# Kernel optimization log

Hardware: AMD Instinct MI355X
Metric: run time of the kernel (lower is better)

Reference implementation:

```python
import jax, jax.numpy as jnp
import numpy as np

# dims
B, N = 8, 16384
MODEL_DIM = 256
F = 32        # feature_dim
H = 4         # num_heads
G = 32        # grid_size
G3 = G * G * G
EPS = 1e-5


def setup_inputs() -> dict:
    key = jax.random.key(0)
    ks = jax.random.split(key, 9)
    eye = jnp.broadcast_to(jnp.eye(3, dtype=jnp.float32), (H, 3, 3))
    return {
        "input_tensor": jax.random.normal(ks[0], (B, MODEL_DIM, N), dtype=jnp.float32),
        "original_points": jax.random.normal(ks[1], (B, 3, N), dtype=jnp.float32),
        # Conv1d kernel_size=1, no bias -> plain (out,in) matmul weight
        "W_kv": jax.random.normal(ks[2], (H * (F + 3), MODEL_DIM), dtype=jnp.float32) * 0.02,
        # key BN affine (orig init weight=0; use small random to exercise path)
        "key_gamma": jax.random.normal(ks[3], (H * 3,), dtype=jnp.float32) * 0.1,
        "key_beta": jax.random.normal(ks[4], (H * 3,), dtype=jnp.float32) * 0.1,
        "val_gamma": 1.0 + jax.random.normal(ks[5], (H * F,), dtype=jnp.float32) * 0.1,
        "val_beta": jax.random.normal(ks[6], (H * F,), dtype=jnp.float32) * 0.1,
        # VolTransformer: per-head affine (rotation-ish matrix + translation)
        "R": eye + jax.random.normal(ks[7], (H, 3, 3), dtype=jnp.float32) * 0.05,
        "t": jax.random.normal(ks[8], (H, 3), dtype=jnp.float32) * 0.1,
    }


def _bn(x, gamma, beta):
    # training-mode BatchNorm1d over (batch, length) per channel; x: (B, C, N)
    mean = jnp.mean(x, axis=(0, 2), keepdims=True)
    var = jnp.var(x, axis=(0, 2), keepdims=True)
    xhat = (x - mean) * jax.lax.rsqrt(var + EPS)
    return xhat * gamma[None, :, None] + beta[None, :, None]


def reference(input_tensor, original_points, W_kv, key_gamma, key_beta,
              val_gamma, val_beta, R, t):
    # 1x1 conv == channel matmul: (B, H*(F+3), N)
    kv = jnp.einsum('om,bmn->bon', W_kv, input_tensor)
    keys_offset = _bn(kv[:, :H * 3], key_gamma, key_beta)          # (B, H*3, N)
    values = _bn(kv[:, H * 3:], val_gamma, val_beta)               # (B, H*F, N)

    keys_offset = keys_offset.reshape(B, H, 3, N)
    pts = original_points[:, None, :, :] + keys_offset             # (B,H,3,N)
    # per-head affine transform (VolTransformer)
    tk = jnp.einsum('hij,bhjn->bhin', R, pts) + t[None, :, :, None]
    lattice = jnp.tanh(tk)                                         # in (-1,1)

    # DifferentiablePositions: map (-1,1) -> [0, G-1], lower corner + local frac
    pos = (lattice + 1.0) * (0.5 * (G - 1))                        # (B,H,3,N)
    idx0 = jnp.clip(jnp.floor(pos), 0.0, G - 2).astype(jnp.int32)  # (B,H,3,N)
    local = pos - idx0                                             # (B,H,3,N)

    values_t = values.reshape(B, H, F, N).transpose(0, 1, 3, 2)    # (B,H,N,F)
    bh_off = (jnp.arange(B * H, dtype=jnp.int32).reshape(B, H) * G3)[:, :, None]

    out = jnp.zeros((B * H * G3, F), dtype=values.dtype)
    # trilinear splat-scatter over the 8 grid corners
    for cx in (0, 1):
        wx = local[:, :, 0] if cx else 1.0 - local[:, :, 0]
        for cy in (0, 1):
            wy = local[:, :, 1] if cy else 1.0 - local[:, :, 1]
            for cz in (0, 1):
                wz = local[:, :, 2] if cz else 1.0 - local[:, :, 2]
                w = wx * wy * wz                                    # (B,H,N)
                flat = ((idx0[:, :, 0] + cx) * G + (idx0[:, :, 1] + cy)) * G \
                       + (idx0[:, :, 2] + cz)                       # (B,H,N)
                seg = (bh_off + flat).reshape(-1)                   # (B*H*N,)
                data = (values_t * w[..., None]).reshape(-1, F)
                out = out + jax.ops.segment_sum(data, seg, num_segments=B * H * G3)

    # (B, H*F, G, G, G)
    return out.reshape(B, H, G3, F).transpose(0, 1, 3, 2).reshape(B, H * F, G, G, G)
```

## Files before the change

### kernel.cpp

```cpp
#include <hip/hip_runtime.h>
#include <cstddef>

#define Bz 8
#define Nn 16384
#define MD 256
#define Ff 32
#define Hh 4
#define Gg 32
#define G3v 32768
#define CKV 140
#define NG 32
#define NBX 31
#define NBY 31
#define NBZ 31
#define NB2 953312
#define NCH 931

using bf16x8 = __attribute__((ext_vector_type(8))) short;
using f32x16 = __attribute__((ext_vector_type(16))) float;

__device__ __forceinline__ unsigned bf16rne(float f) {
    unsigned u = __float_as_uint(f);
    return (u + 0x7fffu + ((u >> 16) & 1u)) >> 16;
}
__device__ __forceinline__ unsigned pk_bf16(float lo, float hi) {
    return bf16rne(lo) | (bf16rne(hi) << 16);
}

__global__ __launch_bounds__(256) void prep_w_kernel(const float* __restrict__ W,
                                                     unsigned short* __restrict__ Wbf)
{
    const int idx = blockIdx.x * 256 + threadIdx.x;
    const int e    = idx & 7;
    const int rest = idx >> 3;
    const int m    = rest % 160;
    const int kg   = rest / 160;
    const int k    = (kg << 3) + e;
    Wbf[idx] = (m < CKV) ? (unsigned short)bf16rne(W[m * MD + k]) : (unsigned short)0;
}

__global__ __launch_bounds__(256, 3) void gemm_stats_kernel(
    const float* __restrict__ X, const unsigned short* __restrict__ Wbf,
    float* __restrict__ vals, float* __restrict__ keys,
    float* __restrict__ gsum, float* __restrict__ gsq)
{
    __shared__ unsigned XlU[4096];
    __shared__ unsigned WlU[5120];
    __shared__ float red[280];

    const int bid = blockIdx.x;
    const int b   = bid >> 7;
    const int n0  = (bid & 127) << 7;
    const int t   = threadIdx.x;
    const int w    = t >> 6;
    const int ln   = t & 31;
    const int hi   = (t >> 5) & 1;

    f32x16 acc[5];
    #pragma unroll
    for (int mt = 0; mt < 5; ++mt)
        #pragma unroll
        for (int j = 0; j < 16; ++j) acc[mt][j] = 0.f;

    for (int ks = 0; ks < 4; ++ks) {
        const int k0 = ks << 6;
        if (ks > 0) __syncthreads();

        #pragma unroll
        for (int it = 0; it < 4; ++it) {
            const int a  = t + (it << 8);
            const int kp = a >> 5;
            const int n4 = (a & 31) << 2;
            const float4 r0 = *reinterpret_cast<const float4*>(
                X + (size_t)(b * MD + k0 + 2 * kp) * Nn + n0 + n4);
            const float4 r1 = *reinterpret_cast<const float4*>(
                X + (size_t)(b * MD + k0 + 2 * kp + 1) * Nn + n0 + n4);
            const int base = ((kp >> 2) << 9) + (n4 << 2) + (kp & 3);
            XlU[base]      = pk_bf16(r0.x, r1.x);
            XlU[base + 4]  = pk_bf16(r0.y, r1.y);
            XlU[base + 8]  = pk_bf16(r0.z, r1.z);
            XlU[base + 12] = pk_bf16(r0.w, r1.w);
        }
        {
            const unsigned* src = reinterpret_cast<const unsigned*>(Wbf) + ks * 5120;
            #pragma unroll
            for (int i = 0; i < 5; ++i) {
                const int d4 = (t + (i << 8)) << 2;
                *reinterpret_cast<uint4*>(&WlU[d4]) =
                    *reinterpret_cast<const uint4*>(&src[d4]);
            }
        }
        __syncthreads();

        const short* xs = reinterpret_cast<const short*>(XlU);
        const short* ws = reinterpret_cast<const short*>(WlU);
        #pragma unroll
        for (int kk = 0; kk < 4; ++kk) {
            const int grp = (kk << 1) + hi;
            const bf16x8 bf = *reinterpret_cast<const bf16x8*>(
                xs + (((grp << 7) + (w << 5) + ln) << 3));
            #pragma unroll
            for (int mt = 0; mt < 5; ++mt) {
                const bf16x8 af = *reinterpret_cast<const bf16x8*>(
                    ws + ((grp * 160 + (mt << 5) + ln) << 3));
                acc[mt] = __builtin_amdgcn_mfma_f32_32x32x16_bf16(af, bf, acc[mt], 0, 0, 0);
            }
        }
    }

    const int n = n0 + (w << 5) + ln;
    #pragma unroll
    for (int mt = 0; mt < 5; ++mt)
        #pragma unroll
        for (int reg = 0; reg < 16; ++reg) {
            const int ml = (reg & 3) + ((reg >> 2) << 3) + (hi << 2);
            const int c  = mt * 32 + ml;
            const float v = acc[mt][reg];
            if (c < 12) {
                const int hh = c / 3, kk2 = c - (c / 3) * 3;
                keys[(size_t)((b * Hh + hh) * 3 + kk2) * Nn + n] = v;
            } else if (c < CKV) {
                const int cv = c - 12;
                vals[((size_t)(b * Hh + (cv >> 5)) * Nn + n) * Ff + (cv & 31)] = v;
            }
        }

    red[t] = 0.f;
    if (t < 24) red[256 + t] = 0.f;
    __syncthreads();
    #pragma unroll
    for (int mt = 0; mt < 5; ++mt)
        #pragma unroll
        for (int reg = 0; reg < 16; ++reg) {
            if (mt == 4 && reg >= 8) continue;
            const int ml = (reg & 3) + ((reg >> 2) << 3) + (hi << 2);
            const int c  = mt * 32 + ml;
            float s = acc[mt][reg];
            float q = s * s;
            #pragma unroll
            for (int off = 1; off < 32; off <<= 1) {
                s += __shfl_xor(s, off);
                q += __shfl_xor(q, off);
            }
            if (ln == 0 && c < CKV) {
                atomicAdd(&red[c], s);
                atomicAdd(&red[140 + c], q);
            }
        }
    __syncthreads();
    if (t < CKV) {
        atomicAdd(&gsum[t], red[t]);
        atomicAdd(&gsq[t],  red[140 + t]);
    }
}

__global__ void finalize_kernel(const float* __restrict__ gsum, const float* __restrict__ gsq,
                                const float* __restrict__ kg, const float* __restrict__ kb,
                                const float* __restrict__ vg, const float* __restrict__ vb,
                                float* __restrict__ scale, float* __restrict__ shift)
{
    const int c = threadIdx.x;
    if (c < CKV) {
        const float inv = 1.f / (float)(Bz * Nn);
        const float m = gsum[c] * inv;
        const float v = fmaf(-m, m, gsq[c] * inv);
        float ga, be;
        if (c < 12) { ga = kg[c]; be = kb[c]; }
        else        { ga = vg[c - 12]; be = vb[c - 12]; }
        const float sc = ga * rsqrtf(v + 1e-5f);
        scale[c] = sc;
        shift[c] = fmaf(-m, sc, be);
    }
}

__global__ __launch_bounds__(256) void points_kernel(
    const float* __restrict__ keys, const float* __restrict__ orig,
    const float* __restrict__ Rm, const float* __restrict__ tv,
    const float* __restrict__ scale, const float* __restrict__ shift,
    float4* __restrict__ rec, int* __restrict__ cnt)
{
    const int bid = blockIdx.x;
    const int g   = bid >> 6;
    const int b   = g >> 2;
    const int h   = g & 3;
    const int t   = threadIdx.x;
    const int n   = ((bid & 63) << 8) + t;

    __shared__ float sR[9], st3[3], ksc[3], ksh[3];
    if (t < 9)       sR[t] = Rm[h * 9 + t];
    else if (t < 12) st3[t - 9] = tv[h * 3 + (t - 9)];
    else if (t < 15) { ksc[t - 12] = scale[h * 3 + (t - 12)];
                       ksh[t - 12] = shift[h * 3 + (t - 12)]; }
    __syncthreads();

    const float k0 = fmaf(keys[(size_t)(g * 3 + 0) * Nn + n], ksc[0], ksh[0]);
    const float k1 = fmaf(keys[(size_t)(g * 3 + 1) * Nn + n], ksc[1], ksh[1]);
    const float k2 = fmaf(keys[(size_t)(g * 3 + 2) * Nn + n], ksc[2], ksh[2]);
    const float p0 = orig[(size_t)(b * 3 + 0) * Nn + n] + k0;
    const float p1 = orig[(size_t)(b * 3 + 1) * Nn + n] + k1;
    const float p2 = orig[(size_t)(b * 3 + 2) * Nn + n] + k2;

    int   idx[3];
    float loc[3];
    #pragma unroll
    for (int d = 0; d < 3; ++d) {
        const float tk = fmaf(sR[d*3+0], p0, fmaf(sR[d*3+1], p1, fmaf(sR[d*3+2], p2, st3[d])));
        const float la = tanhf(tk);
        const float po = (la + 1.f) * 15.5f;
        float fi = floorf(po);
        fi = fminf(fmaxf(fi, 0.f), 30.f);
        idx[d] = (int)fi;
        loc[d] = po - fi;
    }

    const unsigned meta = (unsigned)n | ((unsigned)idx[2] << 14) |
                          ((unsigned)idx[1] << 19) | ((unsigned)idx[0] << 24);
    float4 r;
    r.x = __uint_as_float(meta);
    r.y = loc[0]; r.z = loc[1]; r.w = loc[2];
    rec[(size_t)g * Nn + n] = r;
    const int key = ((g * NBX + idx[0]) * NBY + idx[1]) * NBZ + idx[2];
    atomicAdd(&cnt[key], 1);
}

__global__ __launch_bounds__(256) void scan1_kernel(const int* __restrict__ cnt,
                                                    int* __restrict__ bsum)
{
    __shared__ int s[256];
    const int t = threadIdx.x;
    const int i = blockIdx.x * 1024 + t * 4;
    int v = 0;
    #pragma unroll
    for (int j = 0; j < 4; ++j) { const int idx = i + j; if (idx < NB2) v += cnt[idx]; }
    s[t] = v;
    __syncthreads();
    for (int off = 128; off > 0; off >>= 1) {
        if (t < off) s[t] += s[t + off];
        __syncthreads();
    }
    if (t == 0) bsum[blockIdx.x] = s[0];
}

__global__ __launch_bounds__(1024) void scan2_kernel(const int* __restrict__ bsum,
                                                     int* __restrict__ bscan)
{
    __shared__ int s[1024];
    const int t = threadIdx.x;
    const int v = (t < NCH) ? bsum[t] : 0;
    s[t] = v;
    __syncthreads();
    for (int off = 1; off < 1024; off <<= 1) {
        const int x = (t >= off) ? s[t - off] : 0;
        __syncthreads();
        s[t] += x;
        __syncthreads();
    }
    if (t < NCH) bscan[t] = s[t] - v;
}

__global__ __launch_bounds__(256) void scan3_kernel(const int* __restrict__ cnt,
                                                    const int* __restrict__ bscan,
                                                    int* __restrict__ basep,
                                                    int* __restrict__ cursor)
{
    __shared__ int s[256];
    const int t = threadIdx.x;
    const int i = blockIdx.x * 1024 + t * 4;
    int c[4], l[4];
    int sum = 0;
    #pragma unroll
    for (int j = 0; j < 4; ++j) {
        const int idx = i + j;
        c[j] = (idx < NB2) ? cnt[idx] : 0;
        l[j] = sum; sum += c[j];
    }
    s[t] = sum;
    __syncthreads();
    for (int off = 1; off < 256; off <<= 1) {
        const int x = (t >= off) ? s[t - off] : 0;
        __syncthreads();
        s[t] += x;
        __syncthreads();
    }
    const int off0 = bscan[blockIdx.x] + s[t] - sum;
    #pragma unroll
    for (int j = 0; j < 4; ++j) {
        const int idx = i + j;
        if (idx < NB2) { basep[idx] = off0 + l[j]; cursor[idx] = off0 + l[j]; }
    }
}

__global__ __launch_bounds__(256) void fill_kernel(
    const float4* __restrict__ rec, int* __restrict__ cursor,
    float4* __restrict__ binned)
{
    const int bid = blockIdx.x;
    const int g   = bid >> 6;
    const int t   = threadIdx.x;
    const int n   = ((bid & 63) << 8) + t;
    const float4 r = rec[(size_t)g * Nn + n];
    const unsigned meta = __float_as_uint(r.x);
    const int x0 = (meta >> 24) & 31;
    const int y0 = (meta >> 19) & 31;
    const int z0 = (meta >> 14) & 31;
    const int key = ((g * NBX + x0) * NBY + y0) * NBZ + z0;
    const int pos = atomicAdd(&cursor[key], 1);
    binned[pos] = r;
}

#define PROC(q, vq)                                                          \
{                                                                            \
    const unsigned mq = __float_as_uint((q).x);                              \
    const int zq = (int)((mq >> 14) & 31u);                                  \
    if (zq != zcur) {                                                        \
        if (zcur >= 0) { const int zr = zcur + zc;                           \
                         tg[(zr << 5) + (f ^ zr)] += acc; }                  \
        acc = 0.f; zcur = zq;                                                \
    }                                                                        \
    const int my = (int)((mq >> 19) & 31u);                                  \
    const float wx = dx ? (1.f - (q).y) : (q).y;                             \
    const float wy = (my == y) ? (1.f - (q).z) : (q).z;                      \
    const float wz = zc ? (q).w : (1.f - (q).w);                             \
    acc = fmaf(wx * wy * wz, fmaf(vq, scf, shf), acc);                       \
}

__global__ __launch_bounds__(1024) void gather_kernel(
    const float* __restrict__ vals, const float4* __restrict__ binned,
    const int* __restrict__ basep, const int* __restrict__ cnt,
    const float* __restrict__ scale, const float* __restrict__ shift,
    float* __restrict__ out)
{
    __shared__ float tile[16384];
    __shared__ float sscale[32], sshift[32];

    const int bid = blockIdx.x;
    const int g   = bid & 31;
    const int x   = (bid >> 5) & 31;
    const int yh  = bid >> 10;
    const int h   = g & 3;
    const int t   = threadIdx.x;

    {
        const float4 z4 = make_float4(0.f, 0.f, 0.f, 0.f);
        #pragma unroll
        for (int i = 0; i < 4; ++i)
            *reinterpret_cast<float4*>(&tile[(t << 2) + (i << 12)]) = z4;
    }
    if (t < 32) { sscale[t] = scale[12 + h * 32 + t]; sshift[t] = shift[12 + h * 32 + t]; }
    __syncthreads();

    const int f  = t & 31;
    const int zc = (t >> 5) & 1;
    const int w  = t >> 6;
    const int y  = (yh << 4) + w;
    const float scf = sscale[f], shf = sshift[f];
    const float* vg = vals + ((size_t)g << 19);
    float* const tg = &tile[w << 10];

    float acc = 0.f;
    int zcur = -2;

    const int y0lo = (y > 0)  ? y - 1 : 0;
    const int y0hi = (y < 31) ? y     : 30;

    #pragma unroll
    for (int dx = 0; dx < 2; ++dx) {
        const int x0 = x - 1 + dx;
        if ((unsigned)x0 > 30u) continue;
        const int kb = ((g * NBX + x0) * NBY + y0lo) * NBZ;
        const int ke = ((g * NBX + x0) * NBY + y0hi) * NBZ + 30;
        int r       = basep[kb];
        const int e = basep[ke] + cnt[ke];

        for (; r + 8 <= e; r += 8) {
            const float4 q0 = binned[r];
            const float4 q1 = binned[r + 1];
            const float4 q2 = binned[r + 2];
            const float4 q3 = binned[r + 3];
            const float4 q4 = binned[r + 4];
            const float4 q5 = binned[r + 5];
            const float4 q6 = binned[r + 6];
            const float4 q7 = binned[r + 7];
            const float v0 = vg[((__float_as_uint(q0.x) & 16383u) << 5) + f];
            const float v1 = vg[((__float_as_uint(q1.x) & 16383u) << 5) + f];
            const float v2 = vg[((__float_as_uint(q2.x) & 16383u) << 5) + f];
            const float v3 = vg[((__float_as_uint(q3.x) & 16383u) << 5) + f];
            const float v4 = vg[((__float_as_uint(q4.x) & 16383u) << 5) + f];
            const float v5 = vg[((__float_as_uint(q5.x) & 16383u) << 5) + f];
            const float v6 = vg[((__float_as_uint(q6.x) & 16383u) << 5) + f];
            const float v7 = vg[((__float_as_uint(q7.x) & 16383u) << 5) + f];
            PROC(q0, v0); PROC(q1, v1); PROC(q2, v2); PROC(q3, v3);
            PROC(q4, v4); PROC(q5, v5); PROC(q6, v6); PROC(q7, v7);
        }
        for (; r + 4 <= e; r += 4) {
            const float4 q0 = binned[r];
            const float4 q1 = binned[r + 1];
            const float4 q2 = binned[r + 2];
            const float4 q3 = binned[r + 3];
            const float v0 = vg[((__float_as_uint(q0.x) & 16383u) << 5) + f];
            const float v1 = vg[((__float_as_uint(q1.x) & 16383u) << 5) + f];
            const float v2 = vg[((__float_as_uint(q2.x) & 16383u) << 5) + f];
            const float v3 = vg[((__float_as_uint(q3.x) & 16383u) << 5) + f];
            PROC(q0, v0); PROC(q1, v1); PROC(q2, v2); PROC(q3, v3);
        }
        for (; r < e; ++r) {
            const float4 q0 = binned[r];
            const float v0 = vg[((__float_as_uint(q0.x) & 16383u) << 5) + f];
            PROC(q0, v0);
        }
    }
    if (zcur >= 0) {
        const int zr = zcur + zc;
        tg[(zr << 5) + (f ^ zr)] += acc;
    }
    __syncthreads();

    float* og = out + ((size_t)g << 20) + (x << 10) + (yh << 9);
    #pragma unroll
    for (int i = 0; i < 16; ++i) {
        const int lin = t + (i << 10);
        const int fp  = lin >> 9;
        const int s   = lin & 511;
        const int z   = s & 31;
        og[((size_t)fp << 15) + s] = tile[((s >> 5) << 10) + (z << 5) + (fp ^ z)];
    }
}

__global__ __launch_bounds__(256) void scatter_kernel(
    const float* __restrict__ vals, const float* __restrict__ keys,
    const float* __restrict__ orig, const float* __restrict__ Rm,
    const float* __restrict__ tv, const float* __restrict__ scale,
    const float* __restrict__ shift, float* __restrict__ out)
{
    const int bid   = blockIdx.x;
    const int g     = bid >> 5;
    const int chunk = bid & 31;
    const int b     = g >> 2;
    const int h     = g & 3;

    __shared__ float sc[32], sh[32], sR[9], st3[3], ksc[3], ksh[3];
    const int t = threadIdx.x;
    if (t < 32)      { sc[t] = scale[12 + h * 32 + t]; sh[t] = shift[12 + h * 32 + t]; }
    else if (t < 41) { sR[t - 32]  = Rm[h * 9 + (t - 32)]; }
    else if (t < 44) { st3[t - 41] = tv[h * 3 + (t - 41)]; }
    else if (t < 47) { ksc[t - 44] = scale[h * 3 + (t - 44)];
                       ksh[t - 44] = shift[h * 3 + (t - 44)]; }
    __syncthreads();

    float* const og = out + ((size_t)g << 20);

    #pragma unroll
    for (int pp = 0; pp < 2; ++pp) {
        const int n = (chunk << 9) + (pp << 8) + t;

        const float k0 = fmaf(keys[(size_t)(g * 3 + 0) * Nn + n], ksc[0], ksh[0]);
        const float k1 = fmaf(keys[(size_t)(g * 3 + 1) * Nn + n], ksc[1], ksh[1]);
        const float k2 = fmaf(keys[(size_t)(g * 3 + 2) * Nn + n], ksc[2], ksh[2]);
        const float p0 = orig[(size_t)(b * 3 + 0) * Nn + n] + k0;
        const float p1 = orig[(size_t)(b * 3 + 1) * Nn + n] + k1;
        const float p2 = orig[(size_t)(b * 3 + 2) * Nn + n] + k2;

        int   idx[3];
        float loc[3];
        #pragma unroll
        for (int d = 0; d < 3; ++d) {
            const float tk = fmaf(sR[d*3+0], p0, fmaf(sR[d*3+1], p1, fmaf(sR[d*3+2], p2, st3[d])));
            const float la = tanhf(tk);
            const float po = (la + 1.f) * 15.5f;
            float fi = floorf(po);
            fi = fminf(fmaxf(fi, 0.f), 30.f);
            idx[d] = (int)fi;
            loc[d] = po - fi;
        }
        const int cell = (idx[0] * Gg + idx[1]) * Gg + idx[2];

        float v[32];
        const float4* vp = reinterpret_cast<const float4*>(vals + ((size_t)g * Nn + n) * Ff);
        #pragma unroll
        for (int q = 0; q < 8; ++q) {
            const float4 xq = vp[q];
            v[4*q+0] = fmaf(xq.x, sc[4*q+0], sh[4*q+0]);
            v[4*q+1] = fmaf(xq.y, sc[4*q+1], sh[4*q+1]);
            v[4*q+2] = fmaf(xq.z, sc[4*q+2], sh[4*q+2]);
            v[4*q+3] = fmaf(xq.w, sc[4*q+3], sh[4*q+3]);
        }

        const float wx1 = loc[0], wx0 = 1.f - loc[0];
        const float wy1 = loc[1], wy0 = 1.f - loc[1];
        const float wz1 = loc[2], wz0 = 1.f - loc[2];
        const float cw[8] = { wx0*wy0*wz0, wx0*wy0*wz1, wx0*wy1*wz0, wx0*wy1*wz1,
                              wx1*wy0*wz0, wx1*wy0*wz1, wx1*wy1*wz0, wx1*wy1*wz1 };
        const int  co[8] = { 0, 1, 32, 33, 1024, 1025, 1056, 1057 };

        #pragma unroll
        for (int ff = 0; ff < 32; ++ff) {
            float* const pf = og + (size_t)ff * G3v + cell;
            const float vf = v[ff];
            #pragma unroll
            for (int c8 = 0; c8 < 8; ++c8) {
                atomicAdd(pf + co[c8], cw[c8] * vf);
            }
        }
    }
}

extern "C" void kernel_launch(void* const* d_in, const int* in_sizes, int n_in,
                              void* d_out, int out_size, void* d_ws, size_t ws_size,
                              hipStream_t stream)
{
    const float* X    = (const float*)d_in[0];
    const float* orig = (const float*)d_in[1];
    const float* W    = (const float*)d_in[2];
    const float* kg   = (const float*)d_in[3];
    const float* kb   = (const float*)d_in[4];
    const float* vg   = (const float*)d_in[5];
    const float* vb   = (const float*)d_in[6];
    const float* Rm   = (const float*)d_in[7];
    const float* tv   = (const float*)d_in[8];
    float* out = (float*)d_out;
    float* ws  = (float*)d_ws;

    float* vals  = ws;
    float* keys  = ws + 16777216;
    float* gsum  = ws + 18350080;
    float* gsq   = gsum + 140;
    float* scale = gsum + 280;
    float* shift = scale + 140;
    int*   cnt    = (int*)(ws + 18350848);
    int*   basep  = (int*)(ws + 19304160);
    int*   cursor = (int*)(ws + 20257472);
    int*   bsum   = (int*)(ws + 21210784);
    int*   bscan  = (int*)(ws + 21211808);
    float4* rec    = (float4*)(ws + 21212832);
    float4* binned = (float4*)(ws + 23309984);
    unsigned short* Wbf = (unsigned short*)(ws + 25407136);
    const size_t need_bytes = (size_t)25427616 * sizeof(float);

    hipMemsetAsync(gsum, 0, 280 * sizeof(float), stream);

    prep_w_kernel<<<160, 256, 0, stream>>>(W, Wbf);
    gemm_stats_kernel<<<1024, 256, 0, stream>>>(X, Wbf, vals, keys, gsum, gsq);
    finalize_kernel<<<1, 256, 0, stream>>>(gsum, gsq, kg, kb, vg, vb, scale, shift);

    if (ws_size >= need_bytes) {
        hipMemsetAsync(cnt, 0, (size_t)NB2 * sizeof(int), stream);
        points_kernel<<<2048, 256, 0, stream>>>(keys, orig, Rm, tv, scale, shift, rec, cnt);
        scan1_kernel<<<NCH, 256, 0, stream>>>(cnt, bsum);
        scan2_kernel<<<1, 1024, 0, stream>>>(bsum, bscan);
        scan3_kernel<<<NCH, 256, 0, stream>>>(cnt, bscan, basep, cursor);
        fill_kernel<<<2048, 256, 0, stream>>>(rec, cursor, binned);
        gather_kernel<<<2048, 1024, 0, stream>>>(vals, binned, basep, cnt, scale, shift, out);
    } else {
        hipMemsetAsync(out, 0, (size_t)out_size * sizeof(float), stream);
        scatter_kernel<<<1024, 256, 0, stream>>>(vals, keys, orig, Rm, tv, scale, shift, out);
    }
}
```

Measured before the change: 302.7 us.

## Load GEMM operands directly from global into registers, dropping LDS staging

The GEMM+stats kernel no longer stages X and W tiles through shared memory with barriers. Each lane now reads its eight strided X values straight from global memory, packs them with the HIP bf16 conversion intrinsic, and loads W fragments directly from global or cache. The LDS savings also allow the occupancy hint to rise from 3 to 4 blocks per SM. The cost is that each lane issues scalar 4-byte loads strided by a full row, so coalescing depends on neighbouring lanes, and W is re-read from cache by every wave.

```diff
diff --git a/kernel.cpp b/kernel.cpp
--- a/kernel.cpp
+++ b/kernel.cpp
@@ -1,4 +1,5 @@
 #include <hip/hip_runtime.h>
+#include <hip/hip_bf16.h>
 #include <cstddef>
 
 #define Bz 8
@@ -23,8 +24,11 @@
     unsigned u = __float_as_uint(f);
     return (u + 0x7fffu + ((u >> 16) & 1u)) >> 16;
 }
-__device__ __forceinline__ unsigned pk_bf16(float lo, float hi) {
-    return bf16rne(lo) | (bf16rne(hi) << 16);
+__device__ __forceinline__ unsigned cvt2(float lo, float hi) {
+    __hip_bfloat162 h = __float22bfloat162_rn(make_float2(lo, hi));
+    union { __hip_bfloat162 b; unsigned u; } c;
+    c.b = h;
+    return c.u;
 }
 
 __global__ __launch_bounds__(256) void prep_w_kernel(const float* __restrict__ W,
@@ -39,22 +43,21 @@
     Wbf[idx] = (m < CKV) ? (unsigned short)bf16rne(W[m * MD + k]) : (unsigned short)0;
 }
 
-__global__ __launch_bounds__(256, 3) void gemm_stats_kernel(
+__global__ __launch_bounds__(256, 4) void gemm_stats_kernel(
     const float* __restrict__ X, const unsigned short* __restrict__ Wbf,
     float* __restrict__ vals, float* __restrict__ keys,
     float* __restrict__ gsum, float* __restrict__ gsq)
 {
-    __shared__ unsigned XlU[4096];
-    __shared__ unsigned WlU[5120];
     __shared__ float red[280];
 
     const int bid = blockIdx.x;
     const int b   = bid >> 7;
     const int n0  = (bid & 127) << 7;
     const int t   = threadIdx.x;
-    const int w    = t >> 6;
-    const int ln   = t & 31;
-    const int hi   = (t >> 5) & 1;
+    const int w   = t >> 6;
+    const int ln  = t & 31;
+    const int hi  = (t >> 5) & 1;
+    const int col = n0 + (w << 5) + ln;
 
     f32x16 acc[5];
     #pragma unroll
@@ -62,53 +65,34 @@
         #pragma unroll
         for (int j = 0; j < 16; ++j) acc[mt][j] = 0.f;
 
-    for (int ks = 0; ks < 4; ++ks) {
-        const int k0 = ks << 6;
-        if (ks > 0) __syncthreads();
-
-        #pragma unroll
-        for (int it = 0; it < 4; ++it) {
-            const int a  = t + (it << 8);
-            const int kp = a >> 5;
-            const int n4 = (a & 31) << 2;
-            const float4 r0 = *reinterpret_cast<const float4*>(
-                X + (size_t)(b * MD + k0 + 2 * kp) * Nn + n0 + n4);
-            const float4 r1 = *reinterpret_cast<const float4*>(
-                X + (size_t)(b * MD + k0 + 2 * kp + 1) * Nn + n0 + n4);
-            const int base = ((kp >> 2) << 9) + (n4 << 2) + (kp & 3);
-            XlU[base]      = pk_bf16(r0.x, r1.x);
-            XlU[base + 4]  = pk_bf16(r0.y, r1.y);
-            XlU[base + 8]  = pk_bf16(r0.z, r1.z);
-            XlU[base + 12] = pk_bf16(r0.w, r1.w);
-        }
-        {
-            const unsigned* src = reinterpret_cast<const unsigned*>(Wbf) + ks * 5120;
-            #pragma unroll
-            for (int i = 0; i < 5; ++i) {
-                const int d4 = (t + (i << 8)) << 2;
-                *reinterpret_cast<uint4*>(&WlU[d4]) =
-                    *reinterpret_cast<const uint4*>(&src[d4]);
-            }
-        }
-        __syncthreads();
-
-        const short* xs = reinterpret_cast<const short*>(XlU);
-        const short* ws = reinterpret_cast<const short*>(WlU);
-        #pragma unroll
-        for (int kk = 0; kk < 4; ++kk) {
-            const int grp = (kk << 1) + hi;
-            const bf16x8 bf = *reinterpret_cast<const bf16x8*>(
-                xs + (((grp << 7) + (w << 5) + ln) << 3));
-            #pragma unroll
-            for (int mt = 0; mt < 5; ++mt) {
-                const bf16x8 af = *reinterpret_cast<const bf16x8*>(
-                    ws + ((grp * 160 + (mt << 5) + ln) << 3));
-                acc[mt] = __builtin_amdgcn_mfma_f32_32x32x16_bf16(af, bf, acc[mt], 0, 0, 0);
-            }
-        }
-    }
-
-    const int n = n0 + (w << 5) + ln;
+    const float* Xc = X + (size_t)b * MD * Nn + col;
+
+    #pragma unroll 4
+    for (int kq = 0; kq < 16; ++kq) {
+        const int grp = (kq << 1) + hi;
+        const float* xp = Xc + ((size_t)(grp << 3)) * Nn;
+        const float x0 = xp[0];
+        const float x1 = xp[(size_t)Nn];
+        const float x2 = xp[(size_t)Nn * 2];
+        const float x3 = xp[(size_t)Nn * 3];
+        const float x4 = xp[(size_t)Nn * 4];
+        const float x5 = xp[(size_t)Nn * 5];
+        const float x6 = xp[(size_t)Nn * 6];
+        const float x7 = xp[(size_t)Nn * 7];
+        union { bf16x8 v; unsigned u[4]; } bfu;
+        bfu.u[0] = cvt2(x0, x1);
+        bfu.u[1] = cvt2(x2, x3);
+        bfu.u[2] = cvt2(x4, x5);
+        bfu.u[3] = cvt2(x6, x7);
+        const unsigned short* wp = Wbf + (((size_t)grp * 160) << 3);
+        #pragma unroll
+        for (int mt = 0; mt < 5; ++mt) {
+            const bf16x8 af = *reinterpret_cast<const bf16x8*>(wp + (((mt << 5) + ln) << 3));
+            acc[mt] = __builtin_amdgcn_mfma_f32_32x32x16_bf16(af, bfu.v, acc[mt], 0, 0, 0);
+        }
+    }
+
+    const int n = col;
     #pragma unroll
     for (int mt = 0; mt < 5; ++mt)
         #pragma unroll
```

New measurement: 318.3 us. 1.05x slower.
